# Kernel tuning notes

Hardware: AMD Instinct MI355X
Metric: run time of the kernel (lower is better)

Reference implementation:

```python
import jax, jax.numpy as jnp
import numpy as np

B, C, CI, H, W = 8, 64, 64, 256, 256  # in_channels=64, inter_channels=64, square H=W required by the module's reshapes


def conv1x1(x, w, b):
    # x: [B,Cin,H,W], w: [Cout,Cin], b: [Cout]
    return jnp.einsum('bchw,oc->bohw', x, w) + b[None, :, None, None]


def setup_inputs() -> dict:
    key = jax.random.key(0)
    ks = jax.random.split(key, 10)
    s_in = 1.0 / np.sqrt(C)
    s_int = 1.0 / np.sqrt(CI)
    return {
        'x': jax.random.normal(ks[0], (B, C, H, W), jnp.float32),
        'ref': jax.random.normal(ks[1], (B, C, H, W), jnp.float32),
        'w_g': jax.random.normal(ks[2], (CI, C), jnp.float32) * s_in,
        'b_g': jax.random.normal(ks[3], (CI,), jnp.float32) * s_in,
        'w_theta': jax.random.normal(ks[4], (CI, C), jnp.float32) * s_in,
        'b_theta': jax.random.normal(ks[5], (CI,), jnp.float32) * s_in,
        'w_phi': jax.random.normal(ks[6], (CI, C), jnp.float32) * s_in,
        'b_phi': jax.random.normal(ks[7], (CI,), jnp.float32) * s_in,
        'w_W': jax.random.normal(ks[8], (C, CI), jnp.float32) * s_int,
        'b_W': jax.random.normal(ks[9], (C,), jnp.float32) * s_int,
    }


def reference(x, ref, w_g, b_g, w_theta, b_theta, w_phi, b_phi, w_W, b_W):
    b = x.shape[0]
    h = x.shape[2]
    # 1x1 conv projections then raw row-major reshape [B,Ci,H,W] -> [B, H, Ci*W]
    # (matches torch .view on contiguous NCHW: mixes channel and height indices)
    g_x = conv1x1(x, w_g, b_g).reshape(b, h, -1)          # [B,H,Ci*W]
    theta_x = conv1x1(ref, w_theta, b_theta).reshape(b, h, -1)
    phi_x = conv1x1(x, w_phi, b_phi).reshape(b, h, -1)
    # attention over height: f = theta @ phi^T, softmax over dim=1 (rows, per column)
    f = jnp.einsum('bif,bjf->bij', theta_x, phi_x)        # [B,H,H]
    f_div_C = jax.nn.softmax(f, axis=1)
    y = jnp.einsum('bij,bjf->bif', f_div_C, g_x)          # [B,H,Ci*W]
    y = jnp.transpose(y, (0, 2, 1)).reshape(b, x.shape[1], x.shape[2], h)  # [B,C,H,H]
    W_y = conv1x1(y, w_W, b_W)
    return W_y + x
```

## Files before the change

### kernel.cpp

```cpp
#include <hip/hip_runtime.h>
#include <hip/hip_bf16.h>

#define B_   8
#define C_   64
#define H_   256
#define W_   256
#define HW_  65536
#define CHW  4194304
#define F_   16384
#define KSPLIT 16
#define KCH  1024

typedef __attribute__((ext_vector_type(8)))  short  short8;
typedef __attribute__((ext_vector_type(4)))  float  floatx4;

__device__ __forceinline__ unsigned short f2bf(float v) {
    unsigned int u = __builtin_bit_cast(unsigned int, v);
    unsigned int r = u + 0x7fffu + ((u >> 16) & 1u);
    return (unsigned short)(r >> 16);
}
__device__ __forceinline__ float bf2f(unsigned short h) {
    unsigned int u = ((unsigned int)h) << 16;
    return __builtin_bit_cast(float, u);
}


__global__ __launch_bounds__(256) void prep_kernel(
    const float* __restrict__ w_phi, const float* __restrict__ w_g,
    const float* __restrict__ w_theta, const float* __restrict__ w_W,
    float* __restrict__ wt4)
{
    int tid = threadIdx.x;
    const float* src[4] = {w_phi, w_g, w_theta, w_W};
#pragma unroll
    for (int m = 0; m < 4; ++m) {
        float* dst = wt4 + m * 4096;
        const float* s = src[m];
#pragma unroll
        for (int r = 0; r < 16; ++r) {
            int idx = r * 256 + tid;
            int o = idx >> 6, c = idx & 63;
            dst[c * 64 + o] = s[idx];
        }
    }
}

template<bool RESID>
__global__ __launch_bounds__(256) void g64_kernel(
    const float* __restrict__ in, const float* __restrict__ wt,
    const float* __restrict__ bias, const float* __restrict__ resid,
    float* __restrict__ outp)
{
    __shared__ float sX[16][260];
    __shared__ float sW[16][68];
    int blk = blockIdx.x;
    int b = blk >> 8;
    int p0 = (blk & 255) << 8;
    size_t base = (size_t)b * CHW + p0;
    int tid = threadIdx.x;
    int tp = tid & 31, to = tid >> 5;
    int srow = tid >> 4;
    int scol = (tid & 15) * 4;

    float acc[8][8];
#pragma unroll
    for (int i = 0; i < 8; ++i)
#pragma unroll
        for (int j = 0; j < 8; ++j) acc[i][j] = 0.f;

    for (int c0 = 0; c0 < 64; c0 += 16) {
        float4 xr[4];
#pragma unroll
        for (int r = 0; r < 4; ++r)
            xr[r] = *(const float4*)&in[base + (size_t)(c0 + srow) * HW_ + scol + r * 64];
        float4 wr = *(const float4*)&wt[(c0 + srow) * 64 + scol];
        __syncthreads();
#pragma unroll
        for (int r = 0; r < 4; ++r)
            *(float4*)&sX[srow][scol + r * 64] = xr[r];
        *(float4*)&sW[srow][scol] = wr;
        __syncthreads();
#pragma unroll
        for (int k = 0; k < 16; ++k) {
            float4 x0 = *(const float4*)&sX[k][tp * 4];
            float4 x1 = *(const float4*)&sX[k][128 + tp * 4];
            float4 w0 = *(const float4*)&sW[k][to * 4];
            float4 w1 = *(const float4*)&sW[k][32 + to * 4];
            float xv[8] = {x0.x, x0.y, x0.z, x0.w, x1.x, x1.y, x1.z, x1.w};
            float wv[8] = {w0.x, w0.y, w0.z, w0.w, w1.x, w1.y, w1.z, w1.w};
#pragma unroll
            for (int oo = 0; oo < 8; ++oo)
#pragma unroll
                for (int pp = 0; pp < 8; ++pp)
                    acc[oo][pp] = fmaf(wv[oo], xv[pp], acc[oo][pp]);
        }
    }
#pragma unroll
    for (int oo = 0; oo < 8; ++oo) {
        int o = (oo < 4) ? (to * 4 + oo) : (32 + to * 4 + (oo - 4));
        float bv = bias[o];
        size_t ob0 = base + (size_t)o * HW_ + tp * 4;
        size_t ob1 = ob0 + 128;
        float4 v0 = {acc[oo][0] + bv, acc[oo][1] + bv, acc[oo][2] + bv, acc[oo][3] + bv};
        float4 v1 = {acc[oo][4] + bv, acc[oo][5] + bv, acc[oo][6] + bv, acc[oo][7] + bv};
        if (RESID) {
            float4 r0 = *(const float4*)&resid[ob0];
            float4 r1 = *(const float4*)&resid[ob1];
            v0.x += r0.x; v0.y += r0.y; v0.z += r0.z; v0.w += r0.w;
            v1.x += r1.x; v1.y += r1.y; v1.z += r1.z; v1.w += r1.w;
        }
        *(float4*)&outp[ob0] = v0;
        *(float4*)&outp[ob1] = v1;
    }
}

__global__ __launch_bounds__(256) void fmat_kernel(
    const float* __restrict__ theta, const float* __restrict__ phi,
    float* __restrict__ fpart)
{
    __shared__ unsigned short sPh[128 * 32];
    __shared__ unsigned short sPl[128 * 32];
    __shared__ unsigned short sTh[128 * 32];
    __shared__ unsigned short sTl[128 * 32];

    int blk = blockIdx.x;
    int ks = blk & 15;
    int it = (blk >> 4) & 1;
    int jt = (blk >> 5) & 1;
    int b  = blk >> 6;
    int k0 = ks * KCH;
    int i0 = it * 128, j0 = jt * 128;
    const float* phiB = phi   + (size_t)b * CHW + (size_t)j0 * F_ + k0;
    const float* theB = theta + (size_t)b * CHW + (size_t)i0 * F_ + k0;

    int tid  = threadIdx.x;
    int wave = tid >> 6;
    int lane = tid & 63;
    int wj = wave >> 1, wi = wave & 1;
    int frow = lane & 15;
    int fkq  = lane >> 4;

    int sr = tid >> 2;
    int sk = (tid & 3) * 4;

    floatx4 acc[4][4];
#pragma unroll
    for (int a = 0; a < 4; ++a)
#pragma unroll
        for (int q = 0; q < 4; ++q) acc[a][q] = (floatx4){0.f, 0.f, 0.f, 0.f};

    for (int kk = 0; kk < KCH; kk += 32) {
        float4 pv[4], tv[4];
#pragma unroll
        for (int q = 0; q < 4; ++q) {
            int row = sr + (q & 1) * 64;
            int ko  = sk + (q >> 1) * 16;
            pv[q] = *(const float4*)&phiB[(size_t)row * F_ + kk + ko];
            tv[q] = *(const float4*)&theB[(size_t)row * F_ + kk + ko];
        }
        __syncthreads();
#pragma unroll
        for (int q = 0; q < 4; ++q) {
            int row = sr + (q & 1) * 64;
            int ko  = sk + (q >> 1) * 16;
            int idx = row * 32 + ko;
            float pf[4] = {pv[q].x, pv[q].y, pv[q].z, pv[q].w};
            float tf[4] = {tv[q].x, tv[q].y, tv[q].z, tv[q].w};
            ushort4 ph, pl, th, tl;
            unsigned short* php = (unsigned short*)&ph;
            unsigned short* plp = (unsigned short*)&pl;
            unsigned short* thp = (unsigned short*)&th;
            unsigned short* tlp = (unsigned short*)&tl;
#pragma unroll
            for (int e = 0; e < 4; ++e) {
                unsigned short h = f2bf(pf[e]);
                php[e] = h;
                plp[e] = f2bf(pf[e] - bf2f(h));
                h = f2bf(tf[e]);
                thp[e] = h;
                tlp[e] = f2bf(tf[e] - bf2f(h));
            }
            *(ushort4*)&sPh[idx] = ph;
            *(ushort4*)&sPl[idx] = pl;
            *(ushort4*)&sTh[idx] = th;
            *(ushort4*)&sTl[idx] = tl;
        }
        __syncthreads();

        short8 bh[4], bl[4];
#pragma unroll
        for (int ii = 0; ii < 4; ++ii) {
            int ridx = (wi * 64 + ii * 16 + frow) * 32 + fkq * 8;
            bh[ii] = *(const short8*)&sTh[ridx];
            bl[ii] = *(const short8*)&sTl[ridx];
        }
#pragma unroll
        for (int jj = 0; jj < 4; ++jj) {
            int ridx = (wj * 64 + jj * 16 + frow) * 32 + fkq * 8;
            short8 ah = *(const short8*)&sPh[ridx];
            short8 al = *(const short8*)&sPl[ridx];
#pragma unroll
            for (int ii = 0; ii < 4; ++ii) {
                acc[jj][ii] = __builtin_amdgcn_mfma_f32_16x16x32_bf16(ah, bh[ii], acc[jj][ii], 0, 0, 0);
                acc[jj][ii] = __builtin_amdgcn_mfma_f32_16x16x32_bf16(ah, bl[ii], acc[jj][ii], 0, 0, 0);
                acc[jj][ii] = __builtin_amdgcn_mfma_f32_16x16x32_bf16(al, bh[ii], acc[jj][ii], 0, 0, 0);
            }
        }
    }

    size_t obase = (size_t)(b * KSPLIT + ks) * 65536;
#pragma unroll
    for (int jj = 0; jj < 4; ++jj) {
#pragma unroll
        for (int ii = 0; ii < 4; ++ii) {
            int i = i0 + wi * 64 + ii * 16 + frow;
#pragma unroll
            for (int r = 0; r < 4; ++r) {
                int j = j0 + wj * 64 + jj * 16 + fkq * 4 + r;
                fpart[obase + (size_t)j * 256 + i] = acc[jj][ii][r];
            }
        }
    }
}

__global__ __launch_bounds__(256) void softmax_kernel(
    const float* __restrict__ fpart,
    unsigned short* __restrict__ AtTh,
    unsigned short* __restrict__ AtTl)
{
    __shared__ float red[8];
    int blk = blockIdx.x;
    int b = blk >> 8, j = blk & 255;
    int i = threadIdx.x;
    float v = 0.f;
#pragma unroll
    for (int ks = 0; ks < KSPLIT; ++ks)
        v += fpart[(size_t)(b * KSPLIT + ks) * 65536 + (size_t)j * 256 + i];
    float m = v;
#pragma unroll
    for (int off = 32; off >= 1; off >>= 1) m = fmaxf(m, __shfl_xor(m, off, 64));
    if ((i & 63) == 0) red[i >> 6] = m;
    __syncthreads();
    m = fmaxf(fmaxf(red[0], red[1]), fmaxf(red[2], red[3]));
    float e = __expf(v - m);
    float s = e;
#pragma unroll
    for (int off = 32; off >= 1; off >>= 1) s += __shfl_xor(s, off, 64);
    if ((i & 63) == 0) red[4 + (i >> 6)] = s;
    __syncthreads();
    s = red[4] + red[5] + red[6] + red[7];
    float a = e / s;
    unsigned short h = f2bf(a);
    unsigned short l = f2bf(a - bf2f(h));
    size_t o = (size_t)b * 65536 + (size_t)i * 256 + j;
    AtTh[o] = h;
    AtTl[o] = l;
}

__global__ __launch_bounds__(256) void ymat_kernel(
    const float* __restrict__ g,
    const unsigned short* __restrict__ AtTh,
    const unsigned short* __restrict__ AtTl,
    float* __restrict__ yt)
{
    __shared__ __attribute__((aligned(16))) unsigned short sGh[128 * 40];
    __shared__ __attribute__((aligned(16))) unsigned short sGl[128 * 40];
    __shared__ __attribute__((aligned(16))) unsigned short sAh[128 * 40];
    __shared__ __attribute__((aligned(16))) unsigned short sAl[128 * 40];

    int blk = blockIdx.x;
    int it = blk & 1;
    int Ft = (blk >> 1) & 127;
    int b  = blk >> 8;
    int F0 = Ft * 128;
    int i0 = it * 128;
    const float* gB = g + (size_t)b * CHW + F0;
    const unsigned short* ahB = AtTh + (size_t)b * 65536 + (size_t)i0 * 256;
    const unsigned short* alB = AtTl + (size_t)b * 65536 + (size_t)i0 * 256;

    int tid  = threadIdx.x;
    int wave = tid >> 6;
    int lane = tid & 63;
    int wj = wave >> 1, wi = wave & 1;
    int frow = lane & 15;
    int fkq  = lane >> 4;

    int fq = tid & 31;
    int jq = tid >> 5;
    int ail = tid >> 1;
    int ahf = (tid & 1) * 16;

    floatx4 acc[4][4];
#pragma unroll
    for (int a = 0; a < 4; ++a)
#pragma unroll
        for (int q = 0; q < 4; ++q) acc[a][q] = (floatx4){0.f, 0.f, 0.f, 0.f};

    for (int kk = 0; kk < 256; kk += 32) {
        float4 gv[4];
#pragma unroll
        for (int d = 0; d < 4; ++d)
            gv[d] = *(const float4*)&gB[(size_t)(kk + jq * 4 + d) * F_ + fq * 4];
        short8 a0h = *(const short8*)&ahB[(size_t)ail * 256 + kk + ahf];
        short8 a1h = *(const short8*)&ahB[(size_t)ail * 256 + kk + ahf + 8];
        short8 a0l = *(const short8*)&alB[(size_t)ail * 256 + kk + ahf];
        short8 a1l = *(const short8*)&alB[(size_t)ail * 256 + kk + ahf + 8];
        __syncthreads();

        *(short8*)&sAh[ail * 40 + ahf]     = a0h;
        *(short8*)&sAh[ail * 40 + ahf + 8] = a1h;
        *(short8*)&sAl[ail * 40 + ahf]     = a0l;
        *(short8*)&sAl[ail * 40 + ahf + 8] = a1l;

#pragma unroll
        for (int e = 0; e < 4; ++e) {
            ushort4 hq, lq;
            unsigned short* hp = (unsigned short*)&hq;
            unsigned short* lp = (unsigned short*)&lq;
#pragma unroll
            for (int d = 0; d < 4; ++d) {
                float v = ((const float*)&gv[d])[e];
                unsigned short h = f2bf(v);
                hp[d] = h;
                lp[d] = f2bf(v - bf2f(h));
            }
            int f = fq * 4 + e;
            int off = f * 40 + ((((jq >> 1) ^ (f >> 2)) & 3) << 3) + (jq & 1) * 4;
            *(ushort4*)&sGh[off] = hq;
            *(ushort4*)&sGl[off] = lq;
        }
        __syncthreads();

        short8 bh[4], bl[4];
#pragma unroll
        for (int ii = 0; ii < 4; ++ii) {
            int ridx = (wi * 64 + ii * 16 + frow) * 40 + fkq * 8;
            bh[ii] = *(const short8*)&sAh[ridx];
            bl[ii] = *(const short8*)&sAl[ridx];
        }
#pragma unroll
        for (int jj = 0; jj < 4; ++jj) {
            int f = wj * 64 + jj * 16 + frow;
            int ridx = f * 40 + (((fkq ^ (f >> 2)) & 3) << 3);
            short8 ah = *(const short8*)&sGh[ridx];
            short8 al = *(const short8*)&sGl[ridx];
#pragma unroll
            for (int ii = 0; ii < 4; ++ii) {
                acc[jj][ii] = __builtin_amdgcn_mfma_f32_16x16x32_bf16(ah, bh[ii], acc[jj][ii], 0, 0, 0);
                acc[jj][ii] = __builtin_amdgcn_mfma_f32_16x16x32_bf16(ah, bl[ii], acc[jj][ii], 0, 0, 0);
                acc[jj][ii] = __builtin_amdgcn_mfma_f32_16x16x32_bf16(al, bh[ii], acc[jj][ii], 0, 0, 0);
            }
        }
    }

    size_t ybase = (size_t)b * CHW;
#pragma unroll
    for (int jj = 0; jj < 4; ++jj) {
#pragma unroll
        for (int ii = 0; ii < 4; ++ii) {
            int ig = i0 + wi * 64 + ii * 16 + frow;
#pragma unroll
            for (int r = 0; r < 4; ++r) {
                int Fg = F0 + wj * 64 + jj * 16 + fkq * 4 + r;
                yt[ybase + (size_t)Fg * 256 + ig] = acc[jj][ii][r];
            }
        }
    }
}

extern "C" void kernel_launch(void* const* d_in, const int* in_sizes, int n_in,
                              void* d_out, int out_size, void* d_ws, size_t ws_size,
                              hipStream_t stream) {
    const float* x   = (const float*)d_in[0];
    const float* ref = (const float*)d_in[1];
    const float* w_g = (const float*)d_in[2];
    const float* b_g = (const float*)d_in[3];
    const float* w_t = (const float*)d_in[4];
    const float* b_t = (const float*)d_in[5];
    const float* w_p = (const float*)d_in[6];
    const float* b_p = (const float*)d_in[7];
    const float* w_W = (const float*)d_in[8];
    const float* b_W = (const float*)d_in[9];
    float* out = (float*)d_out;
    float* ws  = (float*)d_ws;

    float* theta = ws;
    float* phi   = ws + 33554432;
    float* g     = ws + 67108864;
    float* yt    = ws;
    float* fpart = ws + 100663296;
    float* wt4   = ws + 109051904;
    float* wt_p  = wt4;
    float* wt_g  = wt4 + 4096;
    float* wt_t  = wt4 + 8192;
    float* wt_W  = wt4 + 12288;
    unsigned short* AtTh = (unsigned short*)(ws + 33554432);
    unsigned short* AtTl = AtTh + 524288;

    prep_kernel<<<1, 256, 0, stream>>>(w_p, w_g, w_t, w_W, wt4);
    g64_kernel<false><<<2048, 256, 0, stream>>>(x,   wt_p, b_p, nullptr, phi);
    g64_kernel<false><<<2048, 256, 0, stream>>>(x,   wt_g, b_g, nullptr, g);
    g64_kernel<false><<<2048, 256, 0, stream>>>(ref, wt_t, b_t, nullptr, theta);
    fmat_kernel<<<512, 256, 0, stream>>>(theta, phi, fpart);
    softmax_kernel<<<2048, 256, 0, stream>>>(fpart, AtTh, AtTl);
    ymat_kernel<<<2048, 256, 0, stream>>>(g, AtTh, AtTl, yt);
    g64_kernel<true><<<2048, 256, 0, stream>>>(yt, wt_W, b_W, x, out);
}
```

Before: 797.5 us.

## Fuse three projection convs into one kernel reusing x tile; pad fmat LDS

Replaces the three separate 1x1-conv launches with one kernel. It loads a 64-channel by 128-pixel tile of x into shared memory once, computes both phi and g from it, then reloads the tile with ref for theta. This removes one full read of x and two launches. The output conv gets a matching single-load variant with 128-pixel tiles, and the fmat kernel's LDS row stride is padded from 32 to 40 to reduce bank conflicts. In exchange, shared memory per block grows to about 51 KB, which may lower occupancy, and each thread's register tile shrinks to 8x4.

```diff
diff --git a/kernel.cpp b/kernel.cpp
--- a/kernel.cpp
+++ b/kernel.cpp
@@ -45,83 +45,140 @@
     }
 }
 
-template<bool RESID>
-__global__ __launch_bounds__(256) void g64_kernel(
-    const float* __restrict__ in, const float* __restrict__ wt,
-    const float* __restrict__ bias, const float* __restrict__ resid,
-    float* __restrict__ outp)
-{
-    __shared__ float sX[16][260];
-    __shared__ float sW[16][68];
-    int blk = blockIdx.x;
-    int b = blk >> 8;
-    int p0 = (blk & 255) << 8;
-    size_t base = (size_t)b * CHW + p0;
-    int tid = threadIdx.x;
-    int tp = tid & 31, to = tid >> 5;
-    int srow = tid >> 4;
-    int scol = (tid & 15) * 4;
-
-    float acc[8][8];
-#pragma unroll
-    for (int i = 0; i < 8; ++i)
-#pragma unroll
-        for (int j = 0; j < 8; ++j) acc[i][j] = 0.f;
-
-    for (int c0 = 0; c0 < 64; c0 += 16) {
-        float4 xr[4];
-#pragma unroll
-        for (int r = 0; r < 4; ++r)
-            xr[r] = *(const float4*)&in[base + (size_t)(c0 + srow) * HW_ + scol + r * 64];
-        float4 wr = *(const float4*)&wt[(c0 + srow) * 64 + scol];
-        __syncthreads();
-#pragma unroll
-        for (int r = 0; r < 4; ++r)
-            *(float4*)&sX[srow][scol + r * 64] = xr[r];
-        *(float4*)&sW[srow][scol] = wr;
-        __syncthreads();
-#pragma unroll
-        for (int k = 0; k < 16; ++k) {
-            float4 x0 = *(const float4*)&sX[k][tp * 4];
-            float4 x1 = *(const float4*)&sX[k][128 + tp * 4];
-            float4 w0 = *(const float4*)&sW[k][to * 4];
-            float4 w1 = *(const float4*)&sW[k][32 + to * 4];
-            float xv[8] = {x0.x, x0.y, x0.z, x0.w, x1.x, x1.y, x1.z, x1.w};
-            float wv[8] = {w0.x, w0.y, w0.z, w0.w, w1.x, w1.y, w1.z, w1.w};
-#pragma unroll
-            for (int oo = 0; oo < 8; ++oo)
-#pragma unroll
-                for (int pp = 0; pp < 8; ++pp)
-                    acc[oo][pp] = fmaf(wv[oo], xv[pp], acc[oo][pp]);
+template<bool HASRES>
+__device__ __forceinline__ void g64_pass(
+    const float (*sX)[132], const float (*sW)[68],
+    int tp, int to, const float* __restrict__ bias,
+    const float* __restrict__ resid, float* __restrict__ outp, size_t base)
+{
+    float4 acc[8];
+#pragma unroll
+    for (int i = 0; i < 8; ++i) acc[i] = (float4){0.f, 0.f, 0.f, 0.f};
+#pragma unroll 8
+    for (int k = 0; k < 64; ++k) {
+        float4 xv = *(const float4*)&sX[k][tp * 4];
+        float4 w0 = *(const float4*)&sW[k][to * 4];
+        float4 w1 = *(const float4*)&sW[k][32 + to * 4];
+        float wv[8] = {w0.x, w0.y, w0.z, w0.w, w1.x, w1.y, w1.z, w1.w};
+#pragma unroll
+        for (int oo = 0; oo < 8; ++oo) {
+            acc[oo].x = fmaf(wv[oo], xv.x, acc[oo].x);
+            acc[oo].y = fmaf(wv[oo], xv.y, acc[oo].y);
+            acc[oo].z = fmaf(wv[oo], xv.z, acc[oo].z);
+            acc[oo].w = fmaf(wv[oo], xv.w, acc[oo].w);
         }
     }
 #pragma unroll
     for (int oo = 0; oo < 8; ++oo) {
         int o = (oo < 4) ? (to * 4 + oo) : (32 + to * 4 + (oo - 4));
         float bv = bias[o];
-        size_t ob0 = base + (size_t)o * HW_ + tp * 4;
-        size_t ob1 = ob0 + 128;
-        float4 v0 = {acc[oo][0] + bv, acc[oo][1] + bv, acc[oo][2] + bv, acc[oo][3] + bv};
-        float4 v1 = {acc[oo][4] + bv, acc[oo][5] + bv, acc[oo][6] + bv, acc[oo][7] + bv};
-        if (RESID) {
-            float4 r0 = *(const float4*)&resid[ob0];
-            float4 r1 = *(const float4*)&resid[ob1];
-            v0.x += r0.x; v0.y += r0.y; v0.z += r0.z; v0.w += r0.w;
-            v1.x += r1.x; v1.y += r1.y; v1.z += r1.z; v1.w += r1.w;
-        }
-        *(float4*)&outp[ob0] = v0;
-        *(float4*)&outp[ob1] = v1;
-    }
-}
-
+        size_t ob = base + (size_t)o * HW_ + tp * 4;
+        float4 v = {acc[oo].x + bv, acc[oo].y + bv, acc[oo].z + bv, acc[oo].w + bv};
+        if (HASRES) {
+            float4 r = *(const float4*)&resid[ob];
+            v.x += r.x; v.y += r.y; v.z += r.z; v.w += r.w;
+        }
+        *(float4*)&outp[ob] = v;
+    }
+}
+
+__global__ __launch_bounds__(256) void g64x3_kernel(
+    const float* __restrict__ x, const float* __restrict__ ref,
+    const float* __restrict__ wt4,
+    const float* __restrict__ b_p, const float* __restrict__ b_g,
+    const float* __restrict__ b_t,
+    float* __restrict__ phi, float* __restrict__ gout,
+    float* __restrict__ theta)
+{
+    __shared__ float sX[64][132];
+    __shared__ float sW[64][68];
+    int blk = blockIdx.x;
+    int b  = blk >> 9;
+    int p0 = (blk & 511) << 7;
+    size_t base = (size_t)b * CHW + p0;
+    int tid  = threadIdx.x;
+    int tp   = tid & 31;
+    int to   = tid >> 5;
+    int srow = tid >> 4;
+    int scol = (tid & 15) * 8;
+    int wrow = tid >> 2;
+    int wcol = (tid & 3) * 16;
+
+#pragma unroll
+    for (int q = 0; q < 4; ++q) {
+        int c = srow + q * 16;
+        const float* sp = &x[base + (size_t)c * HW_ + scol];
+        *(float4*)&sX[c][scol]     = *(const float4*)sp;
+        *(float4*)&sX[c][scol + 4] = *(const float4*)(sp + 4);
+    }
+#pragma unroll
+    for (int q = 0; q < 4; ++q)
+        *(float4*)&sW[wrow][wcol + q * 4] = *(const float4*)&wt4[wrow * 64 + wcol + q * 4];
+    __syncthreads();
+    g64_pass<false>(sX, sW, tp, to, b_p, nullptr, phi, base);
+    __syncthreads();
+#pragma unroll
+    for (int q = 0; q < 4; ++q)
+        *(float4*)&sW[wrow][wcol + q * 4] = *(const float4*)&wt4[4096 + wrow * 64 + wcol + q * 4];
+    __syncthreads();
+    g64_pass<false>(sX, sW, tp, to, b_g, nullptr, gout, base);
+    __syncthreads();
+#pragma unroll
+    for (int q = 0; q < 4; ++q) {
+        int c = srow + q * 16;
+        const float* sp = &ref[base + (size_t)c * HW_ + scol];
+        *(float4*)&sX[c][scol]     = *(const float4*)sp;
+        *(float4*)&sX[c][scol + 4] = *(const float4*)(sp + 4);
+    }
+#pragma unroll
+    for (int q = 0; q < 4; ++q)
+        *(float4*)&sW[wrow][wcol + q * 4] = *(const float4*)&wt4[8192 + wrow * 64 + wcol + q * 4];
+    __syncthreads();
+    g64_pass<false>(sX, sW, tp, to, b_t, nullptr, theta, base);
+}
+
+__global__ __launch_bounds__(256) void g64f_kernel(
+    const float* __restrict__ yt, const float* __restrict__ wtW,
+    const float* __restrict__ bW, const float* __restrict__ resid,
+    float* __restrict__ out)
+{
+    __shared__ float sX[64][132];
+    __shared__ float sW[64][68];
+    int blk = blockIdx.x;
+    int b  = blk >> 9;
+    int p0 = (blk & 511) << 7;
+    size_t base = (size_t)b * CHW + p0;
+    int tid  = threadIdx.x;
+    int tp   = tid & 31;
+    int to   = tid >> 5;
+    int srow = tid >> 4;
+    int scol = (tid & 15) * 8;
+    int wrow = tid >> 2;
+    int wcol = (tid & 3) * 16;
+
+#pragma unroll
+    for (int q = 0; q < 4; ++q) {
+        int c = srow + q * 16;
+        const float* sp = &yt[base + (size_t)c * HW_ + scol];
+        *(float4*)&sX[c][scol]     = *(const float4*)sp;
+        *(float4*)&sX[c][scol + 4] = *(const float4*)(sp + 4);
+    }
+#pragma unroll
+    for (int q = 0; q < 4; ++q)
+        *(float4*)&sW[wrow][wcol + q * 4] = *(const float4*)&wtW[wrow * 64 + wcol + q * 4];
+    __syncthreads();
+    g64_pass<true>(sX, sW, tp, to, bW, resid, out, base);
+}
+
+#define FST 40
 __global__ __launch_bounds__(256) void fmat_kernel(
     const float* __restrict__ theta, const float* __restrict__ phi,
     float* __restrict__ fpart)
 {
-    __shared__ unsigned short sPh[128 * 32];
-    __shared__ unsigned short sPl[128 * 32];
-    __shared__ unsigned short sTh[128 * 32];
-    __shared__ unsigned short sTl[128 * 32];
+    __shared__ unsigned short sPh[128 * FST];
+    __shared__ unsigned short sPl[128 * FST];
+    __shared__ unsigned short sTh[128 * FST];
+    __shared__ unsigned short sTl[128 * FST];
 
     int blk = blockIdx.x;
     int ks = blk & 15;
@@ -163,7 +220,7 @@
         for (int q = 0; q < 4; ++q) {
             int row = sr + (q & 1) * 64;
             int ko  = sk + (q >> 1) * 16;
-            int idx = row * 32 + ko;
+            int idx = row * FST + ko;
             float pf[4] = {pv[q].x, pv[q].y, pv[q].z, pv[q].w};
             float tf[4] = {tv[q].x, tv[q].y, tv[q].z, tv[q].w};
             ushort4 ph, pl, th, tl;
@@ -190,13 +247,13 @@
         short8 bh[4], bl[4];
 #pragma unroll
         for (int ii = 0; ii < 4; ++ii) {
-            int ridx = (wi * 64 + ii * 16 + frow) * 32 + fkq * 8;
+            int ridx = (wi * 64 + ii * 16 + frow) * FST + fkq * 8;
             bh[ii] = *(const short8*)&sTh[ridx];
             bl[ii] = *(const short8*)&sTl[ridx];
         }
 #pragma unroll
         for (int jj = 0; jj < 4; ++jj) {
-            int ridx = (wj * 64 + jj * 16 + frow) * 32 + fkq * 8;
+            int ridx = (wj * 64 + jj * 16 + frow) * FST + fkq * 8;
             short8 ah = *(const short8*)&sPh[ridx];
             short8 al = *(const short8*)&sPl[ridx];
 #pragma unroll
@@ -390,19 +447,14 @@
     float* yt    = ws;
     float* fpart = ws + 100663296;
     float* wt4   = ws + 109051904;
-    float* wt_p  = wt4;
-    float* wt_g  = wt4 + 4096;
-    float* wt_t  = wt4 + 8192;
-    float* wt_W  = wt4 + 12288;
     unsigned short* AtTh = (unsigned short*)(ws + 33554432);
     unsigned short* AtTl = AtTh + 524288;
 
     prep_kernel<<<1, 256, 0, stream>>>(w_p, w_g, w_t, w_W, wt4);
-    g64_kernel<false><<<2048, 256, 0, stream>>>(x,   wt_p, b_p, nullptr, phi);
-    g64_kernel<false><<<2048, 256, 0, stream>>>(x,   wt_g, b_g, nullptr, g);
-    g64_kernel<false><<<2048, 256, 0, stream>>>(ref, wt_t, b_t, nullptr, theta);
+    g64x3_kernel<<<4096, 256, 0, stream>>>(x, ref, wt4, b_p, b_g, b_t,
+                                           phi, g, theta);
     fmat_kernel<<<512, 256, 0, stream>>>(theta, phi, fpart);
     softmax_kernel<<<2048, 256, 0, stream>>>(fpart, AtTh, AtTl);
     ymat_kernel<<<2048, 256, 0, stream>>>(g, AtTh, AtTl, yt);
-    g64_kernel<true><<<2048, 256, 0, stream>>>(yt, wt_W, b_W, x, out);
-}
+    g64f_kernel<<<4096, 256, 0, stream>>>(yt, wt4 + 12288, b_W, x, out);
+}
```

Measured after the change: 710.3 us. -10.9%, faster.
